# Kernel optimization log

Measured on AMD Instinct MI355X. Metric: run time of the kernel, lower is better.

Reference implementation:

```python
import jax, jax.numpy as jnp
import numpy as np

B, T, D = 256, 128, 1024
H = 128          # lstm_hidden
CF = 128         # conv_filters
K = 9            # num_labels
CE_W = 0.2
EPS = 1e-5


def conv1d(x, w, b, pad):
    # x: (B, C, T), w: (O, I, k)
    y = jax.lax.conv_general_dilated(x, w, (1,), [(pad, pad)],
                                     dimension_numbers=('NCH', 'OIH', 'NCH'))
    return y + b[None, :, None]


def batchnorm(x, g, beta):
    # training-mode BN over (N, W) per channel, biased variance (torch default)
    m = x.mean(axis=(0, 2), keepdims=True)
    v = x.var(axis=(0, 2), keepdims=True)
    return (x - m) * jax.lax.rsqrt(v + EPS) * g[None, :, None] + beta[None, :, None]


def lstm_dir(x, Wih, Whh, bih, bhh, reverse):
    # x: (B, T, D_in). PyTorch gate order: i, f, g, o.
    xg = jnp.einsum('btd,gd->btg', x, Wih) + bih + bhh  # (B, T, 4H)
    h0 = jnp.zeros((x.shape[0], Whh.shape[1]), x.dtype)
    c0 = jnp.zeros_like(h0)

    def step(carry, g_t):
        h, c = carry
        gates = g_t + h @ Whh.T
        i, f, g, o = jnp.split(gates, 4, axis=-1)
        c = jax.nn.sigmoid(f) * c + jax.nn.sigmoid(i) * jnp.tanh(g)
        h = jax.nn.sigmoid(o) * jnp.tanh(c)
        return (h, c), h

    _, hs = jax.lax.scan(step, (h0, c0), jnp.swapaxes(xg, 0, 1), reverse=reverse)
    return jnp.swapaxes(hs, 0, 1)  # (B, T, H)


def crf_log_partition(em, mask, start, trans, end):
    # em: (B, T, K), mask: (B, T) bool (mask[:,0] assumed True)
    score = start[None, :] + em[:, 0]  # (B, K)

    def step(score, inp):
        em_t, m_t = inp  # (B, K), (B,)
        nxt = jax.nn.logsumexp(score[:, :, None] + trans[None] + em_t[:, None, :], axis=1)
        return jnp.where(m_t[:, None], nxt, score), None

    score, _ = jax.lax.scan(step, score,
                            (jnp.swapaxes(em[:, 1:], 0, 1), jnp.swapaxes(mask[:, 1:], 0, 1)))
    return jax.nn.logsumexp(score + end[None, :], axis=1)  # (B,)


def crf_numerator(em, tags, mask, start, trans, end):
    mf = mask.astype(em.dtype)
    em_sc = jnp.take_along_axis(em, tags[..., None], axis=-1)[..., 0]  # (B, T)
    tr_sc = trans[tags[:, :-1], tags[:, 1:]]                           # (B, T-1)
    seq_ends = mask.astype(jnp.int32).sum(axis=1) - 1
    last_tags = jnp.take_along_axis(tags, seq_ends[:, None], axis=1)[:, 0]
    return (start[tags[:, 0]] + em_sc[:, 0]
            + ((tr_sc + em_sc[:, 1:]) * mf[:, 1:]).sum(axis=1)
            + end[last_tags])


def setup_inputs() -> dict:
    key = jax.random.key(0)
    ks = jax.random.split(key, 32)
    s = 0.05
    inp = {
        'embeddings': jax.random.normal(ks[0], (B, T, D), jnp.float32),
        'attention_mask': jnp.ones((B, T), jnp.int32),
        'labels': jax.random.randint(ks[1], (B, T), 0, K).astype(jnp.int64),
        'conv5_w': jax.random.normal(ks[2], (CF, D, 5)) * s,
        'conv5_b': jnp.zeros((CF,)),
        'bn1_g': jnp.ones((CF,)),
        'bn1_b': jnp.zeros((CF,)),
        'Wih_f': jax.random.normal(ks[3], (4 * H, CF)) * s,
        'Whh_f': jax.random.normal(ks[4], (4 * H, H)) * s,
        'bih_f': jnp.zeros((4 * H,)),
        'bhh_f': jnp.zeros((4 * H,)),
        'Wih_b': jax.random.normal(ks[5], (4 * H, CF)) * s,
        'Whh_b': jax.random.normal(ks[6], (4 * H, H)) * s,
        'bih_b': jnp.zeros((4 * H,)),
        'bhh_b': jnp.zeros((4 * H,)),
        'conv7_w': jax.random.normal(ks[7], (CF, 2 * H, 7)) * s,
        'conv7_b': jnp.zeros((CF,)),
        'conv9_w': jax.random.normal(ks[8], (CF, 2 * H, 9)) * s,
        'conv9_b': jnp.zeros((CF,)),
        'bn2_g': jnp.ones((2 * CF,)),
        'bn2_b': jnp.zeros((2 * CF,)),
        'cls_w': jax.random.normal(ks[9], (K, 2 * CF)) * s,
        'cls_b': jnp.zeros((K,)),
        'crf_start': jax.random.normal(ks[10], (K,)) * 0.1,
        'crf_trans': jax.random.normal(ks[11], (K, K)) * 0.1,
        'crf_end': jax.random.normal(ks[12], (K,)) * 0.1,
        'class_weights': jax.random.uniform(ks[13], (K,)) + 0.5,
    }
    return inp


def reference(embeddings, attention_mask, labels, conv5_w, conv5_b, bn1_g, bn1_b,
              Wih_f, Whh_f, bih_f, bhh_f, Wih_b, Whh_b, bih_b, bhh_b,
              conv7_w, conv7_b, conv9_w, conv9_b, bn2_g, bn2_b, cls_w, cls_b,
              crf_start, crf_trans, crf_end, class_weights):
    x = embeddings.astype(jnp.float32)
    xt = jnp.swapaxes(x, 1, 2)  # (B, D, T)
    xc = jax.nn.gelu(batchnorm(conv1d(xt, conv5_w, conv5_b, 2), bn1_g, bn1_b),
                     approximate=False)
    xl = jnp.swapaxes(xc, 1, 2)  # (B, T, CF)
    hf = lstm_dir(xl, Wih_f, Whh_f, bih_f, bhh_f, reverse=False)
    hb = lstm_dir(xl, Wih_b, Whh_b, bih_b, bhh_b, reverse=True)
    lstm_out = jnp.swapaxes(jnp.concatenate([hf, hb], axis=-1), 1, 2)  # (B, 2H, T)
    c7 = conv1d(lstm_out, conv7_w, conv7_b, 3)
    c9 = conv1d(lstm_out, conv9_w, conv9_b, 4)
    feat = jax.nn.gelu(batchnorm(jnp.concatenate([c7, c9], axis=1), bn2_g, bn2_b),
                       approximate=False)
    feat = jnp.swapaxes(feat, 1, 2)  # (B, T, 2CF); dropout p=0 -> identity
    logits = jnp.einsum('btf,kf->btk', feat, cls_w) + cls_b  # (B, T, K)

    mask = (attention_mask != 0) & (labels != -100)
    mod_labels = jnp.where(labels == -100, 0, labels).astype(jnp.int32)

    num = crf_numerator(logits, mod_labels, mask, crf_start, crf_trans, crf_end)
    logZ = crf_log_partition(logits, mask, crf_start, crf_trans, crf_end)
    crf_loss = -(num - logZ).mean()

    logp = jax.nn.log_softmax(logits, axis=-1).reshape(-1, K)
    y = labels.reshape(-1)
    valid = y != -100
    yi = jnp.where(valid, y, 0).astype(jnp.int32)
    nll = -jnp.take_along_axis(logp, yi[:, None], axis=1)[:, 0]
    w = jnp.where(valid, class_weights[yi], 0.0)
    ce_loss = (w * nll).sum() / w.sum()

    return (1.0 - CE_W) * crf_loss + CE_W * ce_loss
```

## Files before the change

kernel.cpp:

```cpp
#include <hip/hip_runtime.h>
#include <hip/hip_bf16.h>
#include <math.h>

#define BB 256
#define TT 128
#define DD 1024
#define CFF 128
#define HH 128
#define G4 512
#define NK 9

typedef __attribute__((ext_vector_type(8))) short bf16x8;
typedef __attribute__((ext_vector_type(4))) float f32x4;

__device__ __forceinline__ float bf_lo(unsigned u){ union{unsigned u; float f;} v; v.u = u << 16; return v.f; }
__device__ __forceinline__ float bf_hi(unsigned u){ union{unsigned u; float f;} v; v.u = u & 0xffff0000u; return v.f; }
__device__ __forceinline__ unsigned f2bf(float x){
    union{float f; unsigned u;} v; v.f = x;
    unsigned r = v.u + 0x7fffu + ((v.u >> 16) & 1u);
    return r >> 16;
}
__device__ __forceinline__ float fsig_fast(float x){
    return __builtin_amdgcn_rcpf(1.0f + __builtin_amdgcn_exp2f(-1.44269504f * x));
}
__device__ __forceinline__ float ftanh_fast(float x){
    return 1.0f - 2.0f * __builtin_amdgcn_rcpf(1.0f + __builtin_amdgcn_exp2f(2.88539008f * x));
}
__device__ __forceinline__ float gelu_exact(float x){
    return 0.5f*x*(1.0f + erff(x*0.70710678118654752440f));
}

__global__ __launch_bounds__(256) void prep_convw_kernel(
    const float* __restrict__ w, ushort* __restrict__ Wk,
    int CIN, int KS_SRC, int KS_OUT, int KOFF, int total)
{
    int i = blockIdx.x*256 + threadIdx.x;
    if (i >= total) return;
    int k = i % KS_OUT;
    int d = (i / KS_OUT) % CIN;
    int f = i / (KS_OUT * CIN);
    int ks = k - KOFF;
    float v = (ks >= 0 && ks < KS_SRC) ? w[((size_t)f*CIN + d)*KS_SRC + ks] : 0.f;
    Wk[((size_t)(k*128 + f))*CIN + d] = (ushort)f2bf(v);
}

__global__ __launch_bounds__(256) void prep_xg_kernel(
    const float* __restrict__ Wf, const float* __restrict__ Wb,
    const float* __restrict__ bif, const float* __restrict__ bhf,
    const float* __restrict__ bib, const float* __restrict__ bhb,
    const float* __restrict__ c7b, const float* __restrict__ c9b,
    ushort* __restrict__ Wxg, float* __restrict__ bias_xg, float* __restrict__ cb79)
{
    int i = blockIdx.x*256 + threadIdx.x;
    if (i < 65536) Wxg[i] = (ushort)f2bf(Wf[i]);
    else if (i < 131072) Wxg[i] = (ushort)f2bf(Wb[i - 65536]);
    else if (i < 132096) {
        int j = i - 131072;
        if (j < 512) bias_xg[j] = bif[j] + bhf[j];
        else bias_xg[j] = bib[j-512] + bhb[j-512];
    } else if (i < 132352) {
        int j = i - 132096;
        cb79[j] = (j < 128) ? c7b[j] : c9b[j - 128];
    }
}

template<int CIN, int KS, int KSE_MAX, int SPLIT, bool IN_F32, bool OUT_BF16,
         bool XGT = false, bool CO_BY = false>
__global__ __launch_bounds__(256, 1) void conv_mfma_kernel(
    const void* __restrict__ in_v,
    const ushort* __restrict__ Wk_g,
    const float* __restrict__ bias_g,
    void* __restrict__ outA_v, void* __restrict__ outB_v,
    int OS, int co)
{
    constexpr int PAD = KS / 2;
    constexpr int ROWS = 128 + 2 * PAD;
    constexpr int NSTEP = (SPLIT == 1) ? (CIN / 64) : (CIN / 32);
    constexpr int ATOT = IN_F32 ? ROWS * 8 : ROWS * 4;
    constexpr int BTOT = KSE_MAX * 128 * 4;
    constexpr int AIT = (ATOT + 255) / 256;
    constexpr int BIT = (BTOT + 255) / 256;

    __shared__ ushort A_lds[ROWS * 32];
    __shared__ ushort B_lds[KSE_MAX * 128 * 32];

    const int tid = threadIdx.x;
    const int b   = blockIdx.x;
    const int by  = blockIdx.y;
    const int z   = blockIdx.z;
    const int dbase = (SPLIT == 1) ? z * (CIN / 2) : 0;
    const int k0    = (SPLIT == 2) ? z * KSE_MAX : 0;
    const int kse   = (SPLIT == 2) ? ((z == 0) ? KSE_MAX : (KS - KSE_MAX)) : KS;
    const ushort* __restrict__ Wk = Wk_g + (size_t)by * (size_t)(128 * CIN * KS);
    const float* __restrict__ bias = bias_g + by * 128;
    const int co_eff = co + (CO_BY ? (by << 7) : 0);

    float4 aRf[AIT];
    int4   aRb[AIT];
    int4   bR[BIT];

    auto stage_load = [&](int s) {
        const int d0 = dbase + s * 32;
        if constexpr (IN_F32) {
            const float* __restrict__ inp = (const float*)in_v;
#pragma unroll
            for (int it = 0; it < AIT; ++it) {
                int i = tid + it * 256;
                float4 v = make_float4(0.f, 0.f, 0.f, 0.f);
                if (i < ATOT) {
                    int r = i >> 3, c = i & 7;
                    int t = r - PAD;
                    if (t >= 0 && t < TT)
                        v = *reinterpret_cast<const float4*>(&inp[((size_t)b * TT + t) * CIN + d0 + c * 4]);
                }
                aRf[it] = v;
            }
        } else {
            const ushort* __restrict__ inp = (const ushort*)in_v;
#pragma unroll
            for (int it = 0; it < AIT; ++it) {
                int i = tid + it * 256;
                int4 v = make_int4(0, 0, 0, 0);
                if (i < ATOT) {
                    int r = i >> 2, c = i & 3;
                    int t = r - PAD;
                    if (t >= 0 && t < TT)
                        v = *reinterpret_cast<const int4*>(&inp[((size_t)b * TT + t) * CIN + d0 + c * 8]);
                }
                aRb[it] = v;
            }
        }
#pragma unroll
        for (int it = 0; it < BIT; ++it) {
            int i = tid + it * 256;
            int kk = i >> 9;
            int rem = i & 511;
            int f = rem >> 2, c = rem & 3;
            int4 v = make_int4(0, 0, 0, 0);
            if (kk < kse)
                v = *reinterpret_cast<const int4*>(&Wk[((size_t)((k0 + kk) * 128 + f)) * CIN + d0 + c * 8]);
            bR[it] = v;
        }
    };

    auto stage_write = [&]() {
        if constexpr (IN_F32) {
#pragma unroll
            for (int it = 0; it < AIT; ++it) {
                int i = tid + it * 256;
                if (i < ATOT) {
                    int r = i >> 3, c = i & 7;
                    float4 v = aRf[it];
                    ushort4 h;
                    h.x = (ushort)f2bf(v.x); h.y = (ushort)f2bf(v.y);
                    h.z = (ushort)f2bf(v.z); h.w = (ushort)f2bf(v.w);
                    int slot = (c >> 1) ^ (r & 3);
                    *reinterpret_cast<ushort4*>(&A_lds[r * 32 + slot * 8 + (c & 1) * 4]) = h;
                }
            }
        } else {
#pragma unroll
            for (int it = 0; it < AIT; ++it) {
                int i = tid + it * 256;
                if (i < ATOT) {
                    int r = i >> 2, c = i & 3;
                    int slot = c ^ (r & 3);
                    *reinterpret_cast<int4*>(&A_lds[r * 32 + slot * 8]) = aRb[it];
                }
            }
        }
#pragma unroll
        for (int it = 0; it < BIT; ++it) {
            int i = tid + it * 256;
            int kk = i >> 9;
            int rem = i & 511;
            int f = rem >> 2, c = rem & 3;
            int slot = c ^ (f & 3);
            *reinterpret_cast<int4*>(&B_lds[(kk * 128 + f) * 32 + slot * 8]) = bR[it];
        }
    };

    const int lane = tid & 63;
    const int wave = tid >> 6;
    const int lr = lane & 15;
    const int lk = lane >> 4;
    const int wm = wave >> 1;
    const int wn = wave & 1;

    f32x4 acc[4][4];
#pragma unroll
    for (int m = 0; m < 4; ++m)
#pragma unroll
        for (int n = 0; n < 4; ++n)
            acc[m][n] = (f32x4){0.f, 0.f, 0.f, 0.f};

    stage_load(0);
    stage_write();
    asm volatile("s_waitcnt lgkmcnt(0)" ::: "memory");
    __builtin_amdgcn_s_barrier();
    __builtin_amdgcn_sched_barrier(0);

    for (int s = 0; s < NSTEP; ++s) {
        if (s + 1 < NSTEP) stage_load(s + 1);
#pragma unroll
        for (int kk = 0; kk < KSE_MAX; ++kk) {
            bf16x8 af[4], bfr[4];
#pragma unroll
            for (int m = 0; m < 4; ++m) {
                int R = wm * 64 + m * 16 + lr + k0 + kk;
                if (kk >= kse) R = 0;
                af[m] = *reinterpret_cast<const bf16x8*>(&A_lds[R * 32 + ((lk ^ (R & 3)) * 8)]);
            }
#pragma unroll
            for (int n = 0; n < 4; ++n) {
                int Rb = kk * 128 + wn * 64 + n * 16 + lr;
                bfr[n] = *reinterpret_cast<const bf16x8*>(&B_lds[Rb * 32 + ((lk ^ (lr & 3)) * 8)]);
            }
#pragma unroll
            for (int m = 0; m < 4; ++m)
#pragma unroll
                for (int n = 0; n < 4; ++n)
                    acc[m][n] = __builtin_amdgcn_mfma_f32_16x16x32_bf16(af[m], bfr[n], acc[m][n], 0, 0, 0);
        }
        if (s + 1 < NSTEP) {
            asm volatile("s_waitcnt lgkmcnt(0)" ::: "memory");
            __builtin_amdgcn_s_barrier();
            __builtin_amdgcn_sched_barrier(0);
            stage_write();
            asm volatile("s_waitcnt lgkmcnt(0)" ::: "memory");
            __builtin_amdgcn_s_barrier();
            __builtin_amdgcn_sched_barrier(0);
        }
    }

    const bool addb = (SPLIT == 0) || (z == 0);
    void* out_v = (SPLIT != 0 && z == 1) ? outB_v : outA_v;
    float bv[4];
#pragma unroll
    for (int n = 0; n < 4; ++n) bv[n] = addb ? bias[wn * 64 + n * 16 + lr] : 0.f;
#pragma unroll
    for (int m = 0; m < 4; ++m) {
#pragma unroll
        for (int n = 0; n < 4; ++n) {
            int f = wn * 64 + n * 16 + lr;
#pragma unroll
            for (int q = 0; q < 4; ++q) {
                int trow = wm * 64 + m * 16 + lk * 4 + q;
                float val = acc[m][n][q] + bv[n];
                size_t idx;
                if constexpr (XGT) {
                    int dirg = by >> 2;
                    int g = by & 3;
                    idx = (size_t)dirg * 16777216u + (size_t)trow * 131072u
                        + (size_t)b * 512u + (size_t)(g * 128 + f);
                } else {
                    idx = ((size_t)b * TT + trow) * (size_t)OS + co_eff + f;
                }
                if constexpr (OUT_BF16)
                    ((ushort*)out_v)[idx] = (ushort)f2bf(val);
                else
                    ((float*)out_v)[idx] = val;
            }
        }
    }
}

__global__ __launch_bounds__(256) void bn_stats_kernel(
    const float* __restrict__ y, const float* __restrict__ y2, int C, int rows_per_blk,
    float* __restrict__ sum, float* __restrict__ sqsum)
{
    int tpc = 256 / C;
    int c = threadIdx.x & (C - 1);
    int sub = threadIdx.x / C;
    size_t r0 = (size_t)blockIdx.x * rows_per_blk;
    float s = 0.f, s2 = 0.f;
    for (int r = sub; r < rows_per_blk; r += tpc) {
        size_t i = (r0 + r)*C + c;
        float v = y[i] + y2[i];
        s += v; s2 += v*v;
    }
    __shared__ float ls[256], ls2[256];
    ls[threadIdx.x] = s; ls2[threadIdx.x] = s2;
    __syncthreads();
    if (sub == 0) {
        for (int k = 1; k < tpc; ++k) { s += ls[c + k*C]; s2 += ls2[c + k*C]; }
        atomicAdd(&sum[c], s);
        atomicAdd(&sqsum[c], s2);
    }
}

__global__ __launch_bounds__(256) void bn_gelu_bf16_kernel(
    const float* __restrict__ y, const float* __restrict__ y2,
    const float* __restrict__ sum, const float* __restrict__ sqsum,
    const float* __restrict__ g, const float* __restrict__ beta,
    ushort* __restrict__ out, float inv_n)
{
    size_t i = (size_t)blockIdx.x*256 + threadIdx.x;
    int c = (int)(i & 127);
    float m = sum[c] * inv_n;
    float var = fmaxf(sqsum[c]*inv_n - m*m, 0.f);
    float xv = (y[i] + y2[i] - m) * rsqrtf(var + 1e-5f) * g[c] + beta[c];
    out[i] = (ushort)f2bf(gelu_exact(xv));
}

__global__ __launch_bounds__(512, 1) void lstm_mfma_kernel(
    const ushort* __restrict__ xg2,
    const float* __restrict__ Whhf, const float* __restrict__ Whhb,
    ushort* __restrict__ hfb)
{
    const int tid = threadIdx.x;
    const int lane = tid & 63;
    const int w = tid >> 6;
    const int jc = lane & 15;
    const int kq = lane >> 4;
    const int dir = blockIdx.x >> 4;
    const int b0 = (blockIdx.x & 15) << 4;
    const float* __restrict__ Whh = dir ? Whhb : Whhf;

    bf16x8 Wf[4][4];
#pragma unroll
    for (int g = 0; g < 4; ++g) {
        const float* wr = &Whh[(size_t)((g << 7) + (w << 4) + jc) * HH + (kq << 3)];
#pragma unroll
        for (int s = 0; s < 4; ++s) {
            float4 v0 = *reinterpret_cast<const float4*>(wr + (s << 5));
            float4 v1 = *reinterpret_cast<const float4*>(wr + (s << 5) + 4);
            union { bf16x8 v; ushort u[8]; } pk;
            pk.u[0] = (ushort)f2bf(v0.x); pk.u[1] = (ushort)f2bf(v0.y);
            pk.u[2] = (ushort)f2bf(v0.z); pk.u[3] = (ushort)f2bf(v0.w);
            pk.u[4] = (ushort)f2bf(v1.x); pk.u[5] = (ushort)f2bf(v1.y);
            pk.u[6] = (ushort)f2bf(v1.z); pk.u[7] = (ushort)f2bf(v1.w);
            Wf[g][s] = pk.v;
        }
    }

    __shared__ ushort h_lds[2][16 * 136];
    for (int i = tid; i < 16 * 136; i += 512) h_lds[0][i] = 0;
    f32x4 creg = (f32x4){0.f, 0.f, 0.f, 0.f};

    const ushort* __restrict__ xb = xg2 + (size_t)dir * 16777216u
        + (size_t)(b0 + jc) * 512u + (size_t)((w << 4) + (kq << 2));

    uint2 xA[4], xB[4];
    {
        int tt0 = dir ? (TT - 1) : 0;
        int tt1 = dir ? (TT - 2) : 1;
#pragma unroll
        for (int g = 0; g < 4; ++g) {
            xA[g] = *reinterpret_cast<const uint2*>(xb + (size_t)tt0 * 131072u + (g << 7));
            xB[g] = *reinterpret_cast<const uint2*>(xb + (size_t)tt1 * 131072u + (g << 7));
        }
    }

    __syncthreads();

    int cur = 0;
    const int hrd = jc * 136 + (kq << 3);
    const int col0 = (w << 4) + (kq << 2);

    auto step = [&](int t, uint2 (&xr)[4]) {
        const int tt_c = dir ? (TT - 1 - t) : t;
        f32x4 acc[4];
#pragma unroll
        for (int g = 0; g < 4; ++g) {
            acc[g][0] = bf_lo(xr[g].x);
            acc[g][1] = bf_hi(xr[g].x);
            acc[g][2] = bf_lo(xr[g].y);
            acc[g][3] = bf_hi(xr[g].y);
        }
        {
            int t2 = t + 2; if (t2 >= TT) t2 = TT - 1;
            int ttn = dir ? (TT - 1 - t2) : t2;
#pragma unroll
            for (int g = 0; g < 4; ++g)
                xr[g] = *reinterpret_cast<const uint2*>(xb + (size_t)ttn * 131072u + (g << 7));
        }
        bf16x8 Hf[4];
#pragma unroll
        for (int s = 0; s < 4; ++s)
            Hf[s] = *reinterpret_cast<const bf16x8*>(&h_lds[cur][hrd + (s << 5)]);
#pragma unroll
        for (int s = 0; s < 4; ++s)
#pragma unroll
            for (int g = 0; g < 4; ++g)
                acc[g] = __builtin_amdgcn_mfma_f32_16x16x32_bf16(Wf[g][s], Hf[s], acc[g], 0, 0, 0);
        float hv[4];
#pragma unroll
        for (int r = 0; r < 4; ++r) {
            float iv = fsig_fast(acc[0][r]);
            float fv = fsig_fast(acc[1][r]);
            float gv = ftanh_fast(acc[2][r]);
            float ov = fsig_fast(acc[3][r]);
            float c = fv * creg[r] + iv * gv;
            creg[r] = c;
            hv[r] = ov * ftanh_fast(c);
        }
        ushort4 hb;
        hb.x = (ushort)f2bf(hv[0]); hb.y = (ushort)f2bf(hv[1]);
        hb.z = (ushort)f2bf(hv[2]); hb.w = (ushort)f2bf(hv[3]);
        const int nxt = cur ^ 1;
        *reinterpret_cast<ushort4*>(&h_lds[nxt][jc * 136 + col0]) = hb;
        *reinterpret_cast<ushort4*>(&hfb[((size_t)(b0 + jc) * TT + tt_c) * 256 + (dir << 7) + col0]) = hb;
        asm volatile("s_waitcnt lgkmcnt(0)" ::: "memory");
        __builtin_amdgcn_s_barrier();
        __builtin_amdgcn_sched_barrier(0);
        cur = nxt;
    };

    for (int t = 0; t < TT; t += 2) {
        step(t, xA);
        step(t + 1, xB);
    }
}

__global__ __launch_bounds__(128) void logits_bn_kernel(
    const float* __restrict__ a, const float* __restrict__ bpart,
    const float* __restrict__ sum, const float* __restrict__ sqsum,
    const float* __restrict__ g, const float* __restrict__ beta,
    const float* __restrict__ cw, const float* __restrict__ cb,
    float* __restrict__ lg, float inv_n)
{
    __shared__ float wls[NK*256];
    __shared__ float sc_lds[256], sh_lds[256];
    for (int i = threadIdx.x; i < NK*256; i += 128) wls[i] = cw[i];
    for (int c = threadIdx.x; c < 256; c += 128) {
        float m = sum[c] * inv_n;
        float var = fmaxf(sqsum[c]*inv_n - m*m, 0.f);
        float rs = rsqrtf(var + 1e-5f);
        float s = rs * g[c];
        sc_lds[c] = s;
        sh_lds[c] = beta[c] - m * s;
    }
    __syncthreads();
    size_t row = (size_t)blockIdx.x*128 + threadIdx.x;
    const float* ar = &a[row*256];
    const float* br = &bpart[row*256];
    float acc[NK];
#pragma unroll
    for (int k = 0; k < NK; ++k) acc[k] = 0.f;
    for (int c = 0; c < 256; c += 4) {
        float4 av = *reinterpret_cast<const float4*>(&ar[c]);
        float4 bv = *reinterpret_cast<const float4*>(&br[c]);
        float vv[4] = {av.x + bv.x, av.y + bv.y, av.z + bv.z, av.w + bv.w};
#pragma unroll
        for (int j = 0; j < 4; ++j) {
            float xv = vv[j] * sc_lds[c + j] + sh_lds[c + j];
            float f = gelu_exact(xv);
#pragma unroll
            for (int k = 0; k < NK; ++k)
                acc[k] += f * wls[k*256 + c + j];
        }
    }
#pragma unroll
    for (int k = 0; k < NK; ++k) lg[row*NK + k] = acc[k] + cb[k];
}

__global__ __launch_bounds__(256) void ce_kernel(
    const float* __restrict__ lg, const int* __restrict__ labels,
    const float* __restrict__ cw, float* __restrict__ acc2)
{
    size_t i = (size_t)blockIdx.x*256 + threadIdx.x;
    const float* l = &lg[i*NK];
    float mx = -1e30f;
#pragma unroll
    for (int k = 0; k < NK; ++k) mx = fmaxf(mx, l[k]);
    float se = 0.f;
#pragma unroll
    for (int k = 0; k < NK; ++k) se += expf(l[k] - mx);
    float lz = mx + logf(se);
    int y = labels[i];
    bool valid = (y != -100);
    int yi = valid ? y : 0;
    float nll = lz - l[yi];
    float wv = valid ? cw[yi] : 0.f;
    __shared__ float s1[256], s2[256];
    s1[threadIdx.x] = wv*nll;
    s2[threadIdx.x] = wv;
    __syncthreads();
    for (int s = 128; s > 0; s >>= 1) {
        if (threadIdx.x < s) { s1[threadIdx.x] += s1[threadIdx.x + s]; s2[threadIdx.x] += s2[threadIdx.x + s]; }
        __syncthreads();
    }
    if (threadIdx.x == 0) { atomicAdd(&acc2[0], s1[0]); atomicAdd(&acc2[1], s2[0]); }
}

__global__ __launch_bounds__(64) void crf_kernel(
    const float* __restrict__ lg, const int* __restrict__ att,
    const int* __restrict__ labels, const float* __restrict__ startv,
    const float* __restrict__ trans, const float* __restrict__ endv,
    float* __restrict__ numo, float* __restrict__ logzo)
{
    int b = blockIdx.x;
    int lane = threadIdx.x;
    int lane_c = (lane < NK) ? lane : 0;
    const float* em = &lg[(size_t)b*TT*NK];
    float tr[NK];
#pragma unroll
    for (int i = 0; i < NK; ++i) tr[i] = trans[i*NK + lane_c];
    float score = startv[lane_c] + em[lane_c];

    for (int t = 1; t < TT; ++t) {
        int lt = labels[b*TT + t];
        bool m = (att[b*TT + t] != 0) && (lt != -100);
        float vals[NK];
#pragma unroll
        for (int i = 0; i < NK; ++i)
            vals[i] = __shfl(score, i, 64) + tr[i];
        if (m) {
            float mx = vals[0];
#pragma unroll
            for (int i = 1; i < NK; ++i) mx = fmaxf(mx, vals[i]);
            float sm = 0.f;
#pragma unroll
            for (int i = 0; i < NK; ++i) sm += expf(vals[i] - mx);
            score = mx + logf(sm) + em[t*NK + lane_c];
        }
    }
    float fin = (lane < NK) ? (score + endv[lane_c]) : -1e30f;
    float mx = -1e30f;
#pragma unroll
    for (int i = 0; i < NK; ++i) mx = fmaxf(mx, __shfl(fin, i, 64));
    float sm = 0.f;
#pragma unroll
    for (int i = 0; i < NK; ++i) sm += expf(__shfl(fin, i, 64) - mx);
    if (lane == 0) logzo[b] = mx + logf(sm);

    if (lane == 0) {
        int l0 = labels[b*TT];
        int tag0 = (l0 == -100) ? 0 : l0;
        bool m0 = (att[b*TT] != 0) && (l0 != -100);
        float num = startv[tag0] + em[tag0];
        int prev = tag0;
        int cnt = m0 ? 1 : 0;
        for (int t = 1; t < TT; ++t) {
            int lt = labels[b*TT + t];
            bool m = (att[b*TT + t] != 0) && (lt != -100);
            int tag = (lt == -100) ? 0 : lt;
            if (m) { num += trans[prev*NK + tag] + em[t*NK + tag]; cnt++; }
            prev = tag;
        }
        int le = cnt - 1; if (le < 0) le = 0; if (le >= TT) le = TT - 1;
        int ll = labels[b*TT + le];
        int ltag = (ll == -100) ? 0 : ll;
        num += endv[ltag];
        numo[b] = num;
    }
}

__global__ __launch_bounds__(256) void finalize_kernel(
    const float* __restrict__ numo, const float* __restrict__ logzo,
    const float* __restrict__ acc2, float* __restrict__ out)
{
    __shared__ float red[256];
    int tid = threadIdx.x;
    red[tid] = numo[tid] - logzo[tid];
    __syncthreads();
    for (int s = 128; s > 0; s >>= 1) {
        if (tid < s) red[tid] += red[tid + s];
        __syncthreads();
    }
    if (tid == 0) {
        float crf = -(red[0] / (float)BB);
        float ce = acc2[0] / acc2[1];
        out[0] = 0.8f*crf + 0.2f*ce;
    }
}

extern "C" void kernel_launch(void* const* d_in, const int* in_sizes, int n_in,
                              void* d_out, int out_size, void* d_ws, size_t ws_size,
                              hipStream_t stream)
{
    const float* emb   = (const float*)d_in[0];
    const int*   att   = (const int*)  d_in[1];
    const int*   lab   = (const int*)  d_in[2];
    const float* c5w   = (const float*)d_in[3];
    const float* c5b   = (const float*)d_in[4];
    const float* bn1g  = (const float*)d_in[5];
    const float* bn1b  = (const float*)d_in[6];
    const float* Wihf  = (const float*)d_in[7];
    const float* Whhf  = (const float*)d_in[8];
    const float* bihf  = (const float*)d_in[9];
    const float* bhhf  = (const float*)d_in[10];
    const float* Wihb  = (const float*)d_in[11];
    const float* Whhb  = (const float*)d_in[12];
    const float* bihb  = (const float*)d_in[13];
    const float* bhhb  = (const float*)d_in[14];
    const float* c7w   = (const float*)d_in[15];
    const float* c7b   = (const float*)d_in[16];
    const float* c9w   = (const float*)d_in[17];
    const float* c9b   = (const float*)d_in[18];
    const float* bn2g  = (const float*)d_in[19];
    const float* bn2b  = (const float*)d_in[20];
    const float* clsw  = (const float*)d_in[21];
    const float* clsb  = (const float*)d_in[22];
    const float* cstart= (const float*)d_in[23];
    const float* ctrans= (const float*)d_in[24];
    const float* cend  = (const float*)d_in[25];
    const float* cwts  = (const float*)d_in[26];
    (void)in_sizes; (void)n_in; (void)out_size; (void)ws_size;

    char* wsb = (char*)d_ws;
    size_t off = 0;
    auto alloc = [&](size_t bytes) { void* p = wsb + off; off += (bytes + 255) & ~(size_t)255; return p; };
    float*  y1      = (float*) alloc((size_t)4194304*4);
    ushort* xg      = (ushort*)alloc((size_t)2*16777216*2);
    ushort* hfb     = (ushort*)alloc((size_t)8388608*2);
    ushort* y1h     = (ushort*)alloc((size_t)4194304*2);
    float*  lg      = (float*) alloc((size_t)294912*4);
    ushort* Wk5     = (ushort*)alloc((size_t)655360*2);
    ushort* Wk79    = (ushort*)alloc((size_t)589824*2);
    ushort* Wxg     = (ushort*)alloc((size_t)131072*2);
    float*  bias_xg = (float*) alloc((size_t)1024*4);
    float*  cb79    = (float*) alloc((size_t)256*4);
    float*  stats   = (float*) alloc((size_t)2048*4);
    float* y1b  = (float*)xg;
    float* c79a = (float*)xg;
    float* c79b = (float*)(xg + 16777216);
    float* bn1s = stats;
    float* bn1q = stats + 128;
    float* bn2s = stats + 256;
    float* bn2q = stats + 512;
    float* acc2 = stats + 768;
    float* numo = stats + 770;
    float* logzo = numo + 256;

    hipMemsetAsync(stats, 0, 770*sizeof(float), stream);

    prep_convw_kernel<<<2560, 256, 0, stream>>>(c5w, Wk5, 1024, 5, 5, 0, 655360);
    prep_convw_kernel<<<1152, 256, 0, stream>>>(c7w, Wk79, 256, 7, 9, 1, 294912);
    prep_convw_kernel<<<1152, 256, 0, stream>>>(c9w, Wk79 + 294912, 256, 9, 9, 0, 294912);
    prep_xg_kernel<<<518, 256, 0, stream>>>(Wihf, Wihb, bihf, bhhf, bihb, bhhb, c7b, c9b, Wxg, bias_xg, cb79);

    conv_mfma_kernel<1024,5,5,1,true,false><<<dim3(256,1,2), 256, 0, stream>>>(emb, Wk5, c5b, y1, y1b, 128, 0);
    bn_stats_kernel<<<256, 256, 0, stream>>>(y1, y1b, 128, 128, bn1s, bn1q);
    bn_gelu_bf16_kernel<<<16384, 256, 0, stream>>>(y1, y1b, bn1s, bn1q, bn1g, bn1b, y1h, 1.0f/32768.f);

    conv_mfma_kernel<128,1,1,0,false,true,true><<<dim3(256,8,1), 256, 0, stream>>>(y1h, Wxg, bias_xg, xg, nullptr, 512, 0);
    lstm_mfma_kernel<<<32, 512, 0, stream>>>(xg, Whhf, Whhb, hfb);

    conv_mfma_kernel<256,9,5,2,false,false,false,true><<<dim3(256,2,2), 256, 0, stream>>>(hfb, Wk79, cb79, c79a, c79b, 256, 0);
    bn_stats_kernel<<<256, 256, 0, stream>>>(c79a, c79b, 256, 128, bn2s, bn2q);

    logits_bn_kernel<<<256, 128, 0, stream>>>(c79a, c79b, bn2s, bn2q, bn2g, bn2b, clsw, clsb, lg, 1.0f/32768.f);
    ce_kernel<<<128, 256, 0, stream>>>(lg, lab, cwts, acc2);
    crf_kernel<<<BB, 64, 0, stream>>>(lg, att, lab, cstart, ctrans, cend, numo, logzo);
    finalize_kernel<<<1, 256, 0, stream>>>(numo, logzo, acc2, (float*)d_out);
}
```

Baseline: 481.2 us.

## Split LSTM gate work across twice the waves and merge prep kernels

The LSTM recurrence kernel now runs 16 waves per block instead of 8. Each wave pair splits the four gates: one wave computes the g/o activations and passes them to its partner through LDS, and the partner does the cell update. This halves the MFMA and transcendental work per wave on the serial critical path, at the cost of a second barrier and an LDS round trip every timestep. The four weight-prep launches are also fused into a single kernel to cut launch overhead.

```diff
diff --git a/kernel.cpp b/kernel.cpp
--- a/kernel.cpp
+++ b/kernel.cpp
@@ -30,36 +30,43 @@
     return 0.5f*x*(1.0f + erff(x*0.70710678118654752440f));
 }
 
-__global__ __launch_bounds__(256) void prep_convw_kernel(
-    const float* __restrict__ w, ushort* __restrict__ Wk,
-    int CIN, int KS_SRC, int KS_OUT, int KOFF, int total)
+__global__ __launch_bounds__(256) void prep_all_kernel(
+    const float* __restrict__ c5w, const float* __restrict__ c7w, const float* __restrict__ c9w,
+    const float* __restrict__ Wihf, const float* __restrict__ Wihb,
+    const float* __restrict__ bihf, const float* __restrict__ bhhf,
+    const float* __restrict__ bihb, const float* __restrict__ bhhb,
+    const float* __restrict__ c7b, const float* __restrict__ c9b,
+    ushort* __restrict__ Wk5, ushort* __restrict__ Wk79, ushort* __restrict__ Wxg,
+    float* __restrict__ bias_xg, float* __restrict__ cb79)
 {
     int i = blockIdx.x*256 + threadIdx.x;
-    if (i >= total) return;
-    int k = i % KS_OUT;
-    int d = (i / KS_OUT) % CIN;
-    int f = i / (KS_OUT * CIN);
-    int ks = k - KOFF;
-    float v = (ks >= 0 && ks < KS_SRC) ? w[((size_t)f*CIN + d)*KS_SRC + ks] : 0.f;
-    Wk[((size_t)(k*128 + f))*CIN + d] = (ushort)f2bf(v);
-}
-
-__global__ __launch_bounds__(256) void prep_xg_kernel(
-    const float* __restrict__ Wf, const float* __restrict__ Wb,
-    const float* __restrict__ bif, const float* __restrict__ bhf,
-    const float* __restrict__ bib, const float* __restrict__ bhb,
-    const float* __restrict__ c7b, const float* __restrict__ c9b,
-    ushort* __restrict__ Wxg, float* __restrict__ bias_xg, float* __restrict__ cb79)
-{
-    int i = blockIdx.x*256 + threadIdx.x;
-    if (i < 65536) Wxg[i] = (ushort)f2bf(Wf[i]);
-    else if (i < 131072) Wxg[i] = (ushort)f2bf(Wb[i - 65536]);
-    else if (i < 132096) {
-        int j = i - 131072;
-        if (j < 512) bias_xg[j] = bif[j] + bhf[j];
-        else bias_xg[j] = bib[j-512] + bhb[j-512];
-    } else if (i < 132352) {
-        int j = i - 132096;
+    if (i < 655360) {
+        int k = i % 5, d = (i / 5) & 1023, f = i / 5120;
+        Wk5[((size_t)(k*128 + f))*1024 + d] = (ushort)f2bf(c5w[((size_t)f*1024 + d)*5 + k]);
+    } else if (i < 950272) {
+        int j = i - 655360;
+        int k = j % 9, d = (j / 9) & 255, f = j / 2304;
+        int ks = k - 1;
+        float v = (ks >= 0 && ks < 7) ? c7w[((size_t)f*256 + d)*7 + ks] : 0.f;
+        Wk79[((size_t)(k*128 + f))*256 + d] = (ushort)f2bf(v);
+    } else if (i < 1245184) {
+        int j = i - 950272;
+        int k = j % 9, d = (j / 9) & 255, f = j / 2304;
+        Wk79[294912 + ((size_t)(k*128 + f))*256 + d] = (ushort)f2bf(c9w[((size_t)f*256 + d)*9 + k]);
+    } else if (i < 1310720) {
+        int j = i - 1245184;
+        Wxg[j] = (ushort)f2bf(Wihf[j]);
+    } else if (i < 1376256) {
+        int j = i - 1310720;
+        Wxg[65536 + j] = (ushort)f2bf(Wihb[j]);
+    } else if (i < 1376768) {
+        int j = i - 1376256;
+        bias_xg[j] = bihf[j] + bhhf[j];
+    } else if (i < 1377280) {
+        int j = i - 1376768;
+        bias_xg[512 + j] = bihb[j] + bhhb[j];
+    } else if (i < 1377536) {
+        int j = i - 1377280;
         cb79[j] = (j < 128) ? c7b[j] : c9b[j - 128];
     }
 }
@@ -303,7 +310,7 @@
     out[i] = (ushort)f2bf(gelu_exact(xv));
 }
 
-__global__ __launch_bounds__(512, 1) void lstm_mfma_kernel(
+__global__ __launch_bounds__(1024, 1) void lstm_mfma_kernel(
     const ushort* __restrict__ xg2,
     const float* __restrict__ Whhf, const float* __restrict__ Whhb,
     ushort* __restrict__ hfb)
@@ -311,16 +318,18 @@
     const int tid = threadIdx.x;
     const int lane = tid & 63;
     const int w = tid >> 6;
+    const int w2 = w >> 1;
+    const int gp = w & 1;
     const int jc = lane & 15;
     const int kq = lane >> 4;
     const int dir = blockIdx.x >> 4;
     const int b0 = (blockIdx.x & 15) << 4;
     const float* __restrict__ Whh = dir ? Whhb : Whhf;
 
-    bf16x8 Wf[4][4];
-#pragma unroll
-    for (int g = 0; g < 4; ++g) {
-        const float* wr = &Whh[(size_t)((g << 7) + (w << 4) + jc) * HH + (kq << 3)];
+    bf16x8 Wf[2][4];
+#pragma unroll
+    for (int gg = 0; gg < 2; ++gg) {
+        const float* wr = &Whh[(size_t)(((2*gp + gg) << 7) + (w2 << 4) + jc) * HH + (kq << 3)];
 #pragma unroll
         for (int s = 0; s < 4; ++s) {
             float4 v0 = *reinterpret_cast<const float4*>(wr + (s << 5));
@@ -330,50 +339,53 @@
             pk.u[2] = (ushort)f2bf(v0.z); pk.u[3] = (ushort)f2bf(v0.w);
             pk.u[4] = (ushort)f2bf(v1.x); pk.u[5] = (ushort)f2bf(v1.y);
             pk.u[6] = (ushort)f2bf(v1.z); pk.u[7] = (ushort)f2bf(v1.w);
-            Wf[g][s] = pk.v;
+            Wf[gg][s] = pk.v;
         }
     }
 
     __shared__ ushort h_lds[2][16 * 136];
-    for (int i = tid; i < 16 * 136; i += 512) h_lds[0][i] = 0;
+    __shared__ float  act_lds[16 * 130 * 2];
+    for (int i = tid; i < 16 * 136; i += 1024) h_lds[0][i] = 0;
     f32x4 creg = (f32x4){0.f, 0.f, 0.f, 0.f};
 
+    const int col0 = (w2 << 4) + (kq << 2);
+    const int hrd = jc * 136 + (kq << 3);
+    const int abase = (jc * 130 + col0) * 2;
+
     const ushort* __restrict__ xb = xg2 + (size_t)dir * 16777216u
-        + (size_t)(b0 + jc) * 512u + (size_t)((w << 4) + (kq << 2));
-
-    uint2 xA[4], xB[4];
+        + (size_t)(b0 + jc) * 512u + (size_t)((gp << 8) + col0);
+
+    uint2 xA[2], xB[2];
     {
         int tt0 = dir ? (TT - 1) : 0;
         int tt1 = dir ? (TT - 2) : 1;
 #pragma unroll
-        for (int g = 0; g < 4; ++g) {
-            xA[g] = *reinterpret_cast<const uint2*>(xb + (size_t)tt0 * 131072u + (g << 7));
-            xB[g] = *reinterpret_cast<const uint2*>(xb + (size_t)tt1 * 131072u + (g << 7));
+        for (int gg = 0; gg < 2; ++gg) {
+            xA[gg] = *reinterpret_cast<const uint2*>(xb + (size_t)tt0 * 131072u + (gg << 7));
+            xB[gg] = *reinterpret_cast<const uint2*>(xb + (size_t)tt1 * 131072u + (gg << 7));
         }
     }
 
     __syncthreads();
 
     int cur = 0;
-    const int hrd = jc * 136 + (kq << 3);
-    const int col0 = (w << 4) + (kq << 2);
-
-    auto step = [&](int t, uint2 (&xr)[4]) {
+
+    auto step = [&](int t, uint2 (&xr)[2]) {
         const int tt_c = dir ? (TT - 1 - t) : t;
-        f32x4 acc[4];
-#pragma unroll
-        for (int g = 0; g < 4; ++g) {
-            acc[g][0] = bf_lo(xr[g].x);
-            acc[g][1] = bf_hi(xr[g].x);
-            acc[g][2] = bf_lo(xr[g].y);
-            acc[g][3] = bf_hi(xr[g].y);
+        f32x4 acc[2];
+#pragma unroll
+        for (int gg = 0; gg < 2; ++gg) {
+            acc[gg][0] = bf_lo(xr[gg].x);
+            acc[gg][1] = bf_hi(xr[gg].x);
+            acc[gg][2] = bf_lo(xr[gg].y);
+            acc[gg][3] = bf_hi(xr[gg].y);
         }
         {
             int t2 = t + 2; if (t2 >= TT) t2 = TT - 1;
             int ttn = dir ? (TT - 1 - t2) : t2;
 #pragma unroll
-            for (int g = 0; g < 4; ++g)
-                xr[g] = *reinterpret_cast<const uint2*>(xb + (size_t)ttn * 131072u + (g << 7));
+            for (int gg = 0; gg < 2; ++gg)
+                xr[gg] = *reinterpret_cast<const uint2*>(xb + (size_t)ttn * 131072u + (gg << 7));
         }
         bf16x8 Hf[4];
 #pragma unroll
@@ -382,29 +394,53 @@
 #pragma unroll
         for (int s = 0; s < 4; ++s)
 #pragma unroll
-            for (int g = 0; g < 4; ++g)
-                acc[g] = __builtin_amdgcn_mfma_f32_16x16x32_bf16(Wf[g][s], Hf[s], acc[g], 0, 0, 0);
-        float hv[4];
-#pragma unroll
-        for (int r = 0; r < 4; ++r) {
-            float iv = fsig_fast(acc[0][r]);
-            float fv = fsig_fast(acc[1][r]);
-            float gv = ftanh_fast(acc[2][r]);
-            float ov = fsig_fast(acc[3][r]);
-            float c = fv * creg[r] + iv * gv;
-            creg[r] = c;
-            hv[r] = ov * ftanh_fast(c);
-        }
-        ushort4 hb;
-        hb.x = (ushort)f2bf(hv[0]); hb.y = (ushort)f2bf(hv[1]);
-        hb.z = (ushort)f2bf(hv[2]); hb.w = (ushort)f2bf(hv[3]);
-        const int nxt = cur ^ 1;
-        *reinterpret_cast<ushort4*>(&h_lds[nxt][jc * 136 + col0]) = hb;
-        *reinterpret_cast<ushort4*>(&hfb[((size_t)(b0 + jc) * TT + tt_c) * 256 + (dir << 7) + col0]) = hb;
+            for (int gg = 0; gg < 2; ++gg)
+                acc[gg] = __builtin_amdgcn_mfma_f32_16x16x32_bf16(Wf[gg][s], Hf[s], acc[gg], 0, 0, 0);
+
+        float a0[4], a1[4];
+        if (gp == 1) {
+#pragma unroll
+            for (int r = 0; r < 4; ++r) {
+                a0[r] = ftanh_fast(acc[0][r]);
+                a1[r] = fsig_fast(acc[1][r]);
+            }
+            float4 p0 = make_float4(a0[0], a1[0], a0[1], a1[1]);
+            float4 p1 = make_float4(a0[2], a1[2], a0[3], a1[3]);
+            *reinterpret_cast<float4*>(&act_lds[abase])     = p0;
+            *reinterpret_cast<float4*>(&act_lds[abase + 4]) = p1;
+        } else {
+#pragma unroll
+            for (int r = 0; r < 4; ++r) {
+                a0[r] = fsig_fast(acc[0][r]);
+                a1[r] = fsig_fast(acc[1][r]);
+            }
+        }
         asm volatile("s_waitcnt lgkmcnt(0)" ::: "memory");
         __builtin_amdgcn_s_barrier();
         __builtin_amdgcn_sched_barrier(0);
-        cur = nxt;
+
+        if (gp == 0) {
+            float4 p0 = *reinterpret_cast<const float4*>(&act_lds[abase]);
+            float4 p1 = *reinterpret_cast<const float4*>(&act_lds[abase + 4]);
+            float gv[4] = {p0.x, p0.z, p1.x, p1.z};
+            float ov[4] = {p0.y, p0.w, p1.y, p1.w};
+            float hv[4];
+#pragma unroll
+            for (int r = 0; r < 4; ++r) {
+                float c = a1[r] * creg[r] + a0[r] * gv[r];
+                creg[r] = c;
+                hv[r] = ov[r] * ftanh_fast(c);
+            }
+            ushort4 hb;
+            hb.x = (ushort)f2bf(hv[0]); hb.y = (ushort)f2bf(hv[1]);
+            hb.z = (ushort)f2bf(hv[2]); hb.w = (ushort)f2bf(hv[3]);
+            *reinterpret_cast<ushort4*>(&h_lds[cur ^ 1][jc * 136 + col0]) = hb;
+            *reinterpret_cast<ushort4*>(&hfb[((size_t)(b0 + jc) * TT + tt_c) * 256 + (dir << 7) + col0]) = hb;
+        }
+        asm volatile("s_waitcnt lgkmcnt(0)" ::: "memory");
+        __builtin_amdgcn_s_barrier();
+        __builtin_amdgcn_sched_barrier(0);
+        cur ^= 1;
     };
 
     for (int t = 0; t < TT; t += 2) {
@@ -626,17 +662,15 @@
 
     hipMemsetAsync(stats, 0, 770*sizeof(float), stream);
 
-    prep_convw_kernel<<<2560, 256, 0, stream>>>(c5w, Wk5, 1024, 5, 5, 0, 655360);
-    prep_convw_kernel<<<1152, 256, 0, stream>>>(c7w, Wk79, 256, 7, 9, 1, 294912);
-    prep_convw_kernel<<<1152, 256, 0, stream>>>(c9w, Wk79 + 294912, 256, 9, 9, 0, 294912);
-    prep_xg_kernel<<<518, 256, 0, stream>>>(Wihf, Wihb, bihf, bhhf, bihb, bhhb, c7b, c9b, Wxg, bias_xg, cb79);
+    prep_all_kernel<<<5381, 256, 0, stream>>>(c5w, c7w, c9w, Wihf, Wihb,
+        bihf, bhhf, bihb, bhhb, c7b, c9b, Wk5, Wk79, Wxg, bias_xg, cb79);
 
     conv_mfma_kernel<1024,5,5,1,true,false><<<dim3(256,1,2), 256, 0, stream>>>(emb, Wk5, c5b, y1, y1b, 128, 0);
     bn_stats_kernel<<<256, 256, 0, stream>>>(y1, y1b, 128, 128, bn1s, bn1q);
     bn_gelu_bf16_kernel<<<16384, 256, 0, stream>>>(y1, y1b, bn1s, bn1q, bn1g, bn1b, y1h, 1.0f/32768.f);
 
     conv_mfma_kernel<128,1,1,0,false,true,true><<<dim3(256,8,1), 256, 0, stream>>>(y1h, Wxg, bias_xg, xg, nullptr, 512, 0);
-    lstm_mfma_kernel<<<32, 512, 0, stream>>>(xg, Whhf, Whhb, hfb);
+    lstm_mfma_kernel<<<32, 1024, 0, stream>>>(xg, Whhf, Whhb, hfb);
 
     conv_mfma_kernel<256,9,5,2,false,false,false,true><<<dim3(256,2,2), 256, 0, stream>>>(hfb, Wk79, cb79, c79a, c79b, 256, 0);
     bn_stats_kernel<<<256, 256, 0, stream>>>(c79a, c79b, 256, 128, bn2s, bn2q);
```

Result: slower. 497.9 us (+3.5%).
